# Kernel optimization log

Measured on AMD Instinct MI355X. Metric: run time of the kernel, lower is better.

The kernel has to match this reference:

```python
import jax, jax.numpy as jnp
import numpy as np

NEG_INF = -1e20


def setup_inputs() -> dict:
    key = jax.random.key(0)
    kq, kk, kv, kl = jax.random.split(key, 4)
    B, NQ, NKV, D_QK, D_V = 16, 2048, 2048, 64, 64
    Q_batch = jax.random.normal(kq, (B, NQ, D_QK), dtype=jnp.float32)
    K_batch = jax.random.normal(kk, (B, NKV, D_QK), dtype=jnp.float32)
    V_batch = jax.random.normal(kv, (B, NKV, D_V), dtype=jnp.float32)
    valid_lens = jax.random.randint(kl, (B,), 0, NKV, dtype=jnp.int32)
    return {"Q_batch": Q_batch, "K_batch": K_batch, "V_batch": V_batch,
            "valid_lens": valid_lens}


def reference(Q_batch, K_batch, V_batch, valid_lens):
    d = Q_batch.shape[-1]
    # scores: (B, n_q, n_kv)
    S = jnp.einsum("bqd,bkd->bqk", Q_batch, K_batch) / jnp.sqrt(
        jnp.asarray(d, dtype=Q_batch.dtype))
    n_kv = S.shape[-1]
    # mask kv positions k >= valid_lens[b] (1-D valid_lens broadcast over queries)
    kv_idx = jnp.arange(n_kv)  # (n_kv,)
    mask = kv_idx[None, None, :] < valid_lens[:, None, None]  # (B,1,n_kv)
    S = jnp.where(mask, S, NEG_INF)
    W = jax.nn.softmax(S, axis=-1)
    # dropout rate is 0.0 (eval) -> identity
    return jnp.einsum("bqk,bkv->bqv", W, V_batch)
```

## Files before the change

kernel.cpp:

```cpp
#include <hip/hip_runtime.h>
#include <hip/hip_bf16.h>


typedef __attribute__((ext_vector_type(8))) short short8;
typedef __attribute__((ext_vector_type(4))) float float4v;
typedef __attribute__((ext_vector_type(16))) float f32x16;

#define BATCH 16
#define NQ 2048
#define NKV 2048
#define DH 64
#define KVB 64
#define NTILES (NKV / KVB)
#define TILE_ELEMS (KVB * DH)
#define NEG_INF -1e20f
#define SCALE_LOG2 0.180336880111120f

__device__ __forceinline__ short f2bf(float x) {
    union { float f; unsigned u; } v; v.f = x;
    unsigned r = (v.u + 0x7fffu + ((v.u >> 16) & 1u)) >> 16;
    return (short)r;
}

__device__ __forceinline__ short8 cvt8(float4v a, float4v b) {
    short8 r;
    r[0] = f2bf(a[0]); r[1] = f2bf(a[1]); r[2] = f2bf(a[2]); r[3] = f2bf(a[3]);
    r[4] = f2bf(b[0]); r[5] = f2bf(b[1]); r[6] = f2bf(b[2]); r[7] = f2bf(b[3]);
    return r;
}

__global__ __launch_bounds__(256) void prep_kernel(
    const float* __restrict__ K, const float* __restrict__ V,
    const int* __restrict__ valid_lens,
    short* __restrict__ Kf, short* __restrict__ Vf)
{
    const int b    = blockIdx.x >> 5;
    const int tile = blockIdx.x & 31;
    const int vlen = valid_lens[b];
    const int nkv  = (vlen == 0) ? NKV : vlen;
    if (tile * KVB >= nkv) return;

    const int tid = threadIdx.x;
    const int ln  = tid & 63;
    const int l31 = ln & 31;
    const int hi8 = (ln >> 5) * 8;
    const size_t gbase = ((size_t)b * NKV + (size_t)tile * KVB) * DH;
    short* kt = Kf + (((size_t)b * NTILES + tile) * TILE_ELEMS);
    short* vt = Vf + (((size_t)b * NTILES + tile) * TILE_ELEMS);

#pragma unroll
    for (int s = 0; s < 2; ++s) {
        const int kk = tid >> 6;
        const int kv = s * 32 + l31;
        const int d  = kk * 16 + hi8;
        const float* p = K + gbase + (size_t)kv * DH + d;
        *reinterpret_cast<short8*>(kt + (s * 256 + tid) * 8) =
            cvt8(*reinterpret_cast<const float4v*>(p),
                 *reinterpret_cast<const float4v*>(p + 4));
    }
#pragma unroll
    for (int t = 0; t < 2; ++t) {
        const int ks  = tid >> 6;
        const int d   = t * 32 + l31;
        const int kv0 = ks * 16 + hi8;
        short8 w;
#pragma unroll
        for (int j = 0; j < 8; ++j)
            w[j] = f2bf(V[gbase + (size_t)(kv0 + j) * DH + d]);
        *reinterpret_cast<short8*>(vt + (t * 256 + tid) * 8) = w;
    }
}

__global__ __launch_bounds__(512) void attn_fwd_kernel(
    const float* __restrict__ Q,
    const short* __restrict__ Kf,
    const short* __restrict__ Vf,
    const int* __restrict__ valid_lens,
    float* __restrict__ O)
{
    __shared__ float  mrg[4][2048];
    __shared__ float2 mlb[4][32];

    const int tid  = threadIdx.x;
    const int wave = tid >> 6;
    const int lane = tid & 63;
    const int l31  = lane & 31;
    const int hi   = lane >> 5;
    const int h    = wave >> 2;
    const int qsub = wave & 3;

    const int b  = blockIdx.x & 15;
    const int qt = blockIdx.x >> 4;
    const int qbase = qt * 128 + qsub * 32;

    const int vlen  = valid_lens[b];
    const int nkv   = (vlen == 0) ? NKV : vlen;
    const int tiles = (nkv + KVB - 1) / KVB;
    const int nh = (tiles + 1 - h) >> 1;

    const float* Qb = Q + ((size_t)b * NQ + qbase + l31) * DH;
    short8 qfrag[4];
#pragma unroll
    for (int kk = 0; kk < 4; ++kk) {
        const float* p = Qb + kk * 16 + hi * 8;
        float4v a = *reinterpret_cast<const float4v*>(p);
        float4v c = *reinterpret_cast<const float4v*>(p + 4);
#pragma unroll
        for (int j = 0; j < 4; ++j) { a[j] *= SCALE_LOG2; c[j] *= SCALE_LOG2; }
        qfrag[kk] = cvt8(a, c);
    }

    const short* Kfb = Kf + (size_t)b * NTILES * TILE_ELEMS + lane * 8;
    const short* Vfb = Vf + (size_t)b * NTILES * TILE_ELEMS + lane * 8;

    auto load_k = [&](short8 (&kf)[8], int tile) {
        const short* p = Kfb + (size_t)tile * TILE_ELEMS;
#pragma unroll
        for (int i = 0; i < 8; ++i)
            kf[i] = *reinterpret_cast<const short8*>(p + i * 512);
    };
    auto load_v = [&](short8 (&vf)[8], int tile) {
        const short* p = Vfb + (size_t)tile * TILE_ELEMS;
#pragma unroll
        for (int i = 0; i < 8; ++i)
            vf[i] = *reinterpret_cast<const short8*>(p + i * 512);
    };

    f32x16 acc_o[2];
#pragma unroll
    for (int t = 0; t < 2; ++t)
#pragma unroll
        for (int r = 0; r < 16; ++r) acc_o[t][r] = 0.f;
    float m = -INFINITY, lsum = 0.f;

    short8 kf0[8], kf1[8], vfr[8];

    auto body = [&](short8 (&kc)[8], short8 (&kn)[8], int it) {
        const int tile = 2 * it + h;
        load_v(vfr, tile);

        f32x16 acs[2];
#pragma unroll
        for (int s = 0; s < 2; ++s)
#pragma unroll
            for (int r = 0; r < 16; ++r) acs[s][r] = 0.f;
        __builtin_amdgcn_s_setprio(1);
#pragma unroll
        for (int s = 0; s < 2; ++s)
#pragma unroll
            for (int kk = 0; kk < 4; ++kk)
                acs[s] = __builtin_amdgcn_mfma_f32_32x32x16_bf16(
                    kc[s * 4 + kk], qfrag[kk], acs[s], 0, 0, 0);
        __builtin_amdgcn_s_setprio(0);

        if (it + 1 < nh) load_k(kn, 2 * (it + 1) + h);

        const int kvb0 = tile * KVB + 4 * hi;
#pragma unroll
        for (int s = 0; s < 2; ++s) {
            const int vlim = vlen - (kvb0 + s * 32);
#pragma unroll
            for (int r = 0; r < 16; ++r) {
                const int rc = (r & 3) + 8 * (r >> 2);
                acs[s][r] = (rc < vlim) ? acs[s][r] : NEG_INF;
            }
        }

        float mx[8];
#pragma unroll
        for (int r = 0; r < 8; ++r)
            mx[r] = fmaxf(fmaxf(acs[0][r], acs[0][r + 8]),
                          fmaxf(acs[1][r], acs[1][r + 8]));
#pragma unroll
        for (int d = 4; d; d >>= 1)
#pragma unroll
            for (int r = 0; r < d; ++r) mx[r] = fmaxf(mx[r], mx[r + d]);
        float x = mx[0];
        x = fmaxf(x, __shfl_xor(x, 32, 64));

        float mn = m;
        if (!__all(x <= m + 8.f)) {
            mn = fmaxf(m, x);
            const float alpha = exp2f(m - mn);
            m = mn;
            lsum *= alpha;
#pragma unroll
            for (int r = 0; r < 16; ++r) {
                const int rc = (r & 3) + 8 * (r >> 2);
                const float ar = __shfl(alpha, rc + 4 * hi, 64);
                acc_o[0][r] *= ar;
                acc_o[1][r] *= ar;
            }
        }

#pragma unroll
        for (int s = 0; s < 2; ++s)
#pragma unroll
            for (int r = 0; r < 16; ++r) acs[s][r] = exp2f(acs[s][r] - mn);
        float sm[8];
#pragma unroll
        for (int r = 0; r < 8; ++r)
            sm[r] = (acs[0][r] + acs[0][r + 8]) + (acs[1][r] + acs[1][r + 8]);
#pragma unroll
        for (int d = 4; d; d >>= 1)
#pragma unroll
            for (int r = 0; r < d; ++r) sm[r] += sm[r + d];
        float rs = sm[0];
        rs += __shfl_xor(rs, 32, 64);
        lsum += rs;

        unsigned pk[2][4][2];
#pragma unroll
        for (int s = 0; s < 2; ++s)
#pragma unroll
            for (int be = 0; be < 4; ++be)
#pragma unroll
                for (int c = 0; c < 2; ++c)
                    asm("v_cvt_pk_bf16_f32 %0, %1, %2"
                        : "=v"(pk[s][be][c])
                        : "v"(acs[s][4 * be + 2 * c]),
                          "v"(acs[s][4 * be + 2 * c + 1]));

        __builtin_amdgcn_s_setprio(1);
#pragma unroll
        for (int ks = 0; ks < 4; ++ks) {
            const int s = ks >> 1, g = ks & 1;
            unsigned w0 = pk[s][2 * g][0], w2 = pk[s][2 * g + 1][0];
            unsigned w1 = pk[s][2 * g][1], w3 = pk[s][2 * g + 1][1];
            asm("v_permlane32_swap_b32 %0, %1" : "+v"(w0), "+v"(w2));
            asm("v_permlane32_swap_b32 %0, %1" : "+v"(w1), "+v"(w3));
            union { unsigned u[4]; short8 s8; } pf;
            pf.u[0] = w0; pf.u[1] = w1; pf.u[2] = w2; pf.u[3] = w3;
#pragma unroll
            for (int t = 0; t < 2; ++t)
                acc_o[t] = __builtin_amdgcn_mfma_f32_32x32x16_bf16(
                    pf.s8, vfr[t * 4 + ks], acc_o[t], 0, 0, 0);
        }
        __builtin_amdgcn_s_setprio(0);
    };

    if (nh > 0) load_k(kf0, h);
    int it = 0;
    for (; it + 1 < nh; it += 2) {
        body(kf0, kf1, it);
        body(kf1, kf0, it + 1);
    }
    if (it < nh) body(kf0, kf1, it);

    if (h == 1) {
#pragma unroll
        for (int t = 0; t < 2; ++t)
#pragma unroll
            for (int r = 0; r < 16; ++r)
                mrg[qsub][(t * 16 + r) * 64 + lane] = acc_o[t][r];
        if (lane < 32) mlb[qsub][lane] = float2{m, lsum};
    }
    __syncthreads();
    if (h == 0) {
        const float2 o1 = mlb[qsub][l31];
        const float m1 = o1.x, l1 = o1.y;
        const float M  = (l1 > 0.f) ? fmaxf(m, m1) : m;
        const float w0 = exp2f(m - M);
        const float w1 = (l1 > 0.f) ? exp2f(m1 - M) : 0.f;
        const float L  = lsum * w0 + l1 * w1;
        const float a0 = w0 / L, a1 = w1 / L;
        float* Ob = O + ((size_t)b * NQ + qbase) * DH;
#pragma unroll
        for (int r = 0; r < 16; ++r) {
            const int rc = (r & 3) + 8 * (r >> 2);
            const float a0r = __shfl(a0, rc + 4 * hi, 64);
            const float a1r = __shfl(a1, rc + 4 * hi, 64);
#pragma unroll
            for (int t = 0; t < 2; ++t) {
                const float oh = mrg[qsub][(t * 16 + r) * 64 + lane];
                Ob[(size_t)(rc + 4 * hi) * DH + t * 32 + l31] =
                    acc_o[t][r] * a0r + oh * a1r;
            }
        }
    }
}

extern "C" void kernel_launch(void* const* d_in, const int* in_sizes, int n_in,
                              void* d_out, int out_size, void* d_ws, size_t ws_size,
                              hipStream_t stream) {
    const float* Q = (const float*)d_in[0];
    const float* K = (const float*)d_in[1];
    const float* V = (const float*)d_in[2];
    const int* vl  = (const int*)d_in[3];
    float* Out     = (float*)d_out;

    short* Kws = (short*)d_ws;
    short* Vws = Kws + (size_t)BATCH * NTILES * TILE_ELEMS;

    prep_kernel<<<dim3(BATCH * NTILES), dim3(256), 0, stream>>>(K, V, vl, Kws, Vws);
    attn_fwd_kernel<<<dim3(BATCH * (NQ / 128)), dim3(512), 0, stream>>>(
        Q, Kws, Vws, vl, Out);
}
```

Baseline: 43.85 us.

## Coalesce V prep, split output accumulators, skip unneeded masking, use raw v_exp

The prep kernel now reads V as float4 rows and scatters short4 chunks into the transposed layout, replacing scalar strided loads. The attention loop alternates between two output accumulator sets so consecutive PV MFMA chains are independent, and sums them at the end. Masking now runs only on tiles that cross valid_len, and exp2f is replaced by the raw v_exp_f32 instruction. In exchange, the extra accumulators raise register pressure, and v_exp skips the denormal handling that exp2f provides.

```diff
diff --git a/kernel.cpp b/kernel.cpp
--- a/kernel.cpp
+++ b/kernel.cpp
@@ -3,6 +3,7 @@
 
 
 typedef __attribute__((ext_vector_type(8))) short short8;
+typedef __attribute__((ext_vector_type(4))) short short4v;
 typedef __attribute__((ext_vector_type(4))) float float4v;
 typedef __attribute__((ext_vector_type(16))) float f32x16;
 
@@ -27,6 +28,10 @@
     r[0] = f2bf(a[0]); r[1] = f2bf(a[1]); r[2] = f2bf(a[2]); r[3] = f2bf(a[3]);
     r[4] = f2bf(b[0]); r[5] = f2bf(b[1]); r[6] = f2bf(b[2]); r[7] = f2bf(b[3]);
     return r;
+}
+
+__device__ __forceinline__ float fexp2(float x) {
+    float r; asm("v_exp_f32 %0, %1" : "=v"(r) : "v"(x)); return r;
 }
 
 __global__ __launch_bounds__(256) void prep_kernel(
@@ -58,16 +63,27 @@
             cvt8(*reinterpret_cast<const float4v*>(p),
                  *reinterpret_cast<const float4v*>(p + 4));
     }
-#pragma unroll
-    for (int t = 0; t < 2; ++t) {
-        const int ks  = tid >> 6;
-        const int d   = t * 32 + l31;
-        const int kv0 = ks * 16 + hi8;
-        short8 w;
-#pragma unroll
-        for (int j = 0; j < 8; ++j)
-            w[j] = f2bf(V[gbase + (size_t)(kv0 + j) * DH + d]);
-        *reinterpret_cast<short8*>(vt + (t * 256 + tid) * 8) = w;
+    {
+        const int kv0 = (tid >> 4) << 2;
+        const int d0  = (tid & 15) << 2;
+        const float* p = V + gbase + (size_t)kv0 * DH + d0;
+        float4v r0 = *reinterpret_cast<const float4v*>(p);
+        float4v r1 = *reinterpret_cast<const float4v*>(p + DH);
+        float4v r2 = *reinterpret_cast<const float4v*>(p + 2 * DH);
+        float4v r3 = *reinterpret_cast<const float4v*>(p + 3 * DH);
+        const int ks  = kv0 >> 4;
+        const int hiv = (kv0 >> 3) & 1;
+        const int j0  = kv0 & 7;
+#pragma unroll
+        for (int k = 0; k < 4; ++k) {
+            const int d    = d0 + k;
+            const int lanev = (d & 31) + 32 * hiv;
+            short4v w;
+            w[0] = f2bf(r0[k]); w[1] = f2bf(r1[k]);
+            w[2] = f2bf(r2[k]); w[3] = f2bf(r3[k]);
+            *reinterpret_cast<short4v*>(
+                vt + (((d >> 5) * 4 + ks) * 64 + lanev) * 8 + j0) = w;
+        }
     }
 }
 
@@ -119,25 +135,26 @@
         for (int i = 0; i < 8; ++i)
             kf[i] = *reinterpret_cast<const short8*>(p + i * 512);
     };
-    auto load_v = [&](short8 (&vf)[8], int tile) {
-        const short* p = Vfb + (size_t)tile * TILE_ELEMS;
-#pragma unroll
-        for (int i = 0; i < 8; ++i)
-            vf[i] = *reinterpret_cast<const short8*>(p + i * 512);
-    };
-
-    f32x16 acc_o[2];
+
+    f32x16 acc_oA[2], acc_oB[2];
 #pragma unroll
     for (int t = 0; t < 2; ++t)
 #pragma unroll
-        for (int r = 0; r < 16; ++r) acc_o[t][r] = 0.f;
+        for (int r = 0; r < 16; ++r) { acc_oA[t][r] = 0.f; acc_oB[t][r] = 0.f; }
     float m = -INFINITY, lsum = 0.f;
 
-    short8 kf0[8], kf1[8], vfr[8];
-
-    auto body = [&](short8 (&kc)[8], short8 (&kn)[8], int it) {
+    short8 kf0[8], kf1[8];
+
+    auto body = [&](short8 (&kc)[8], short8 (&kn)[8], f32x16 (&am)[2], int it) {
         const int tile = 2 * it + h;
-        load_v(vfr, tile);
+
+        short8 vfr[8];
+        {
+            const short* p = Vfb + (size_t)tile * TILE_ELEMS;
+#pragma unroll
+            for (int i = 0; i < 8; ++i)
+                vfr[i] = *reinterpret_cast<const short8*>(p + i * 512);
+        }
 
         f32x16 acs[2];
 #pragma unroll
@@ -155,14 +172,16 @@
 
         if (it + 1 < nh) load_k(kn, 2 * (it + 1) + h);
 
-        const int kvb0 = tile * KVB + 4 * hi;
-#pragma unroll
-        for (int s = 0; s < 2; ++s) {
-            const int vlim = vlen - (kvb0 + s * 32);
-#pragma unroll
-            for (int r = 0; r < 16; ++r) {
-                const int rc = (r & 3) + 8 * (r >> 2);
-                acs[s][r] = (rc < vlim) ? acs[s][r] : NEG_INF;
+        if (vlen < (tile + 1) * KVB) {
+            const int kvb0 = tile * KVB + 4 * hi;
+#pragma unroll
+            for (int s = 0; s < 2; ++s) {
+                const int vlim = vlen - (kvb0 + s * 32);
+#pragma unroll
+                for (int r = 0; r < 16; ++r) {
+                    const int rc = (r & 3) + 8 * (r >> 2);
+                    acs[s][r] = (rc < vlim) ? acs[s][r] : NEG_INF;
+                }
             }
         }
 
@@ -181,22 +200,22 @@
         float mn = m;
         if (!__all(x <= m + 8.f)) {
             mn = fmaxf(m, x);
-            const float alpha = exp2f(m - mn);
+            const float alpha = fexp2(m - mn);
             m = mn;
             lsum *= alpha;
 #pragma unroll
             for (int r = 0; r < 16; ++r) {
                 const int rc = (r & 3) + 8 * (r >> 2);
                 const float ar = __shfl(alpha, rc + 4 * hi, 64);
-                acc_o[0][r] *= ar;
-                acc_o[1][r] *= ar;
+                acc_oA[0][r] *= ar; acc_oA[1][r] *= ar;
+                acc_oB[0][r] *= ar; acc_oB[1][r] *= ar;
             }
         }
 
 #pragma unroll
         for (int s = 0; s < 2; ++s)
 #pragma unroll
-            for (int r = 0; r < 16; ++r) acs[s][r] = exp2f(acs[s][r] - mn);
+            for (int r = 0; r < 16; ++r) acs[s][r] = fexp2(acs[s][r] - mn);
         float sm[8];
 #pragma unroll
         for (int r = 0; r < 8; ++r)
@@ -233,8 +252,8 @@
             pf.u[0] = w0; pf.u[1] = w1; pf.u[2] = w2; pf.u[3] = w3;
 #pragma unroll
             for (int t = 0; t < 2; ++t)
-                acc_o[t] = __builtin_amdgcn_mfma_f32_32x32x16_bf16(
-                    pf.s8, vfr[t * 4 + ks], acc_o[t], 0, 0, 0);
+                am[t] = __builtin_amdgcn_mfma_f32_32x32x16_bf16(
+                    pf.s8, vfr[t * 4 + ks], am[t], 0, 0, 0);
         }
         __builtin_amdgcn_s_setprio(0);
     };
@@ -242,17 +261,22 @@
     if (nh > 0) load_k(kf0, h);
     int it = 0;
     for (; it + 1 < nh; it += 2) {
-        body(kf0, kf1, it);
-        body(kf1, kf0, it + 1);
-    }
-    if (it < nh) body(kf0, kf1, it);
+        body(kf0, kf1, acc_oA, it);
+        body(kf1, kf0, acc_oB, it + 1);
+    }
+    if (it < nh) body(kf0, kf1, acc_oA, it);
+
+#pragma unroll
+    for (int t = 0; t < 2; ++t)
+#pragma unroll
+        for (int r = 0; r < 16; ++r) acc_oA[t][r] += acc_oB[t][r];
 
     if (h == 1) {
 #pragma unroll
         for (int t = 0; t < 2; ++t)
 #pragma unroll
             for (int r = 0; r < 16; ++r)
-                mrg[qsub][(t * 16 + r) * 64 + lane] = acc_o[t][r];
+                mrg[qsub][(t * 16 + r) * 64 + lane] = acc_oA[t][r];
         if (lane < 32) mlb[qsub][lane] = float2{m, lsum};
     }
     __syncthreads();
@@ -260,8 +284,8 @@
         const float2 o1 = mlb[qsub][l31];
         const float m1 = o1.x, l1 = o1.y;
         const float M  = (l1 > 0.f) ? fmaxf(m, m1) : m;
-        const float w0 = exp2f(m - M);
-        const float w1 = (l1 > 0.f) ? exp2f(m1 - M) : 0.f;
+        const float w0 = fexp2(m - M);
+        const float w1 = (l1 > 0.f) ? fexp2(m1 - M) : 0.f;
         const float L  = lsum * w0 + l1 * w1;
         const float a0 = w0 / L, a1 = w1 / L;
         float* Ob = O + ((size_t)b * NQ + qbase) * DH;
@@ -274,7 +298,7 @@
             for (int t = 0; t < 2; ++t) {
                 const float oh = mrg[qsub][(t * 16 + r) * 64 + lane];
                 Ob[(size_t)(rc + 4 * hi) * DH + t * 32 + l31] =
-                    acc_o[t][r] * a0r + oh * a1r;
+                    acc_oA[t][r] * a0r + oh * a1r;
             }
         }
     }
```

Measured after the change: 35.09 us. 20.0% less time.
